# Kernel optimization log

Measured on AMD Instinct MI355X. Metric: run time of the kernel, lower is better.

## Reference

```python
import jax, jax.numpy as jnp
import numpy as np

# dims
BB, T, D_IN = 16, 2048, 64
D = 512          # hidden_dim (d_model)
DI = 2 * D       # d_inner (expand=2)
N = 16           # d_state
DC = 4           # d_conv
R = D // 16      # dt_rank = 32
L = 3            # n_layer
D_OUT = 128


def setup_inputs() -> dict:
    key = jax.random.key(0)
    ks = jax.random.split(key, 10)
    g = lambda k, shape, s: (jax.random.normal(k, shape, jnp.float32) * s)
    A_log = jnp.tile(jnp.log(jnp.arange(1, N + 1, dtype=jnp.float32))[None, None, :], (L, DI, 1))
    return {
        "x": g(ks[0], (BB, T, D_IN), 1.0),
        "Wi": g(ks[1], (D, D_IN), 0.05), "bi": jnp.zeros((D,), jnp.float32),
        "Win": g(ks[2], (L, 2 * DI, D), 0.02),
        "convw": g(ks[3], (L, DI, DC), 0.2), "convb": jnp.zeros((L, DI), jnp.float32),
        "Wx": g(ks[4], (L, R + 2 * N, DI), 0.02),
        "Wdt": g(ks[5], (L, DI, R), 0.05), "bdt": jnp.full((L, DI), -1.0, jnp.float32),
        "A_log": A_log, "Dp": jnp.ones((L, DI), jnp.float32),
        "Wout": g(ks[6], (L, D, DI), 0.02),
        "Wo": g(ks[7], (D_OUT, D), 0.05), "bo": jnp.zeros((D_OUT,), jnp.float32),
    }


def _selective_scan(u, delta, A, Bm, Cm, Dv):
    # u, delta: [B,T,DI]; A: [DI,N]; Bm, Cm: [B,T,N]; Dv: [DI]
    def step(h, inp):
        d_t, u_t, B_t, C_t = inp  # [B,DI],[B,DI],[B,N],[B,N]
        dA = jnp.exp(d_t[:, :, None] * A)                      # [B,DI,N]
        h = dA * h + (d_t * u_t)[:, :, None] * B_t[:, None, :]  # [B,DI,N]
        y = jnp.einsum('bdn,bn->bd', h, C_t)
        return h, y

    h0 = jnp.zeros((u.shape[0], u.shape[2], A.shape[1]), u.dtype)
    xs = (delta.transpose(1, 0, 2), u.transpose(1, 0, 2),
          Bm.transpose(1, 0, 2), Cm.transpose(1, 0, 2))
    _, ys = jax.lax.scan(step, h0, xs)
    return ys.transpose(1, 0, 2) + u * Dv


def _mamba_layer(x, Win, cw, cb, Wx, Wdt, bdt, A_log, Dv, Wout):
    xz = x @ Win.T                      # [B,T,2*DI]
    xin, z = jnp.split(xz, 2, axis=-1)
    # causal depthwise conv1d
    xc = jax.lax.conv_general_dilated(
        xin.transpose(0, 2, 1), cw[:, None, :], (1,), [(DC - 1, 0)],
        feature_group_count=DI, dimension_numbers=('NCH', 'OIH', 'NCH'))
    u = jax.nn.silu((xc + cb[None, :, None]).transpose(0, 2, 1))  # [B,T,DI]
    dbc = u @ Wx.T                      # [B,T,R+2N]
    dt, Bm, Cm = dbc[..., :R], dbc[..., R:R + N], dbc[..., R + N:]
    delta = jax.nn.softplus(dt @ Wdt.T + bdt)
    A = -jnp.exp(A_log)
    y = _selective_scan(u, delta, A, Bm, Cm, Dv)
    return (y * jax.nn.silu(z)) @ Wout.T


def reference(x, Wi, bi, Win, convw, convb, Wx, Wdt, bdt, A_log, Dp, Wout, Wo, bo):
    h = x @ Wi.T + bi
    for l in range(L):
        h = _mamba_layer(h, Win[l], convw[l], convb[l], Wx[l], Wdt[l], bdt[l],
                         A_log[l], Dp[l], Wout[l])
    return jnp.tanh(h @ Wo.T + bo)  # [B,T,output_dim]
```

## Files before the change

### kernel.cpp

```cpp
#include <hip/hip_runtime.h>
#include <hip/hip_bf16.h>

#define BB_ 16
#define T_ 2048
#define DIN_ 64
#define D_ 512
#define DI_ 1024
#define N_ 16
#define DC_ 4
#define R_ 32
#define L_ 3
#define DOUT_ 128
#define CL_ 64
#define NCH_ (T_ / CL_)

typedef __attribute__((ext_vector_type(8))) _Float16 f16x8;
typedef __attribute__((ext_vector_type(4))) float f32x4;

__device__ __forceinline__ float silu_f(float x) { return x / (1.f + __expf(-x)); }

__device__ __forceinline__ float softplus_f(float t) {
    return fmaxf(t, 0.f) + __logf(1.f + __expf(-fabsf(t)));
}

__device__ __forceinline__ unsigned short f2h(float f) {
    union { _Float16 h; unsigned short u; } c;
    c.h = (_Float16)f;
    return c.u;
}

__device__ __forceinline__ float h2f(unsigned short u) {
    union { unsigned short u; _Float16 h; } c;
    c.u = u;
    return (float)c.h;
}

__device__ __forceinline__ void gload_lds16(const unsigned short* g,
                                            unsigned short* l) {
    __builtin_amdgcn_global_load_lds(
        (const __attribute__((address_space(1))) void*)g,
        (__attribute__((address_space(3))) void*)l, 16, 0, 0);
}

__device__ __forceinline__ float decode_scale(unsigned int bits) {
    if (bits == 0u) return 1.f;
    const int E = (int)(bits >> 23) & 0xFF;
    return __uint_as_float((unsigned)(265 - E) << 23);
}

__device__ __forceinline__ uint4 pack8(float4 lo, float4 hi, float s) {
    union { uint4 u; unsigned short h[8]; } r;
    r.h[0] = f2h(lo.x * s); r.h[1] = f2h(lo.y * s);
    r.h[2] = f2h(lo.z * s); r.h[3] = f2h(lo.w * s);
    r.h[4] = f2h(hi.x * s); r.h[5] = f2h(hi.y * s);
    r.h[6] = f2h(hi.z * s); r.h[7] = f2h(hi.w * s);
    return r.u;
}

__device__ __forceinline__ const float* wregion(
    int r, const float* Win, const float* Wout, const float* Wx,
    const float* Wo, size_t* n4)
{
    if (r < 3)       { *n4 = 262144; return Win  + (size_t)r * 1048576; }
    else if (r < 6)  { *n4 = 131072; return Wout + (size_t)(r - 3) * 524288; }
    else if (r == 6) { *n4 = 16384;  return Wo; }
    else             { *n4 = 16384;  return Wx  + (size_t)(r - 7) * 65536; }
}

__global__ __launch_bounds__(256) void amax_all(
    const float* __restrict__ Win, const float* __restrict__ Wout,
    const float* __restrict__ Wx, const float* __restrict__ Wo,
    unsigned int* __restrict__ scales)
{
    size_t n4;
    const float* p = wregion(blockIdx.z, Win, Wout, Wx, Wo, &n4);
    float m = 0.f;
    for (size_t i = (size_t)blockIdx.x * 256 + threadIdx.x; i < n4;
         i += (size_t)gridDim.x * 256) {
        const float4 v = ((const float4*)p)[i];
        m = fmaxf(m, fmaxf(fmaxf(fabsf(v.x), fabsf(v.y)),
                           fmaxf(fabsf(v.z), fabsf(v.w))));
    }
#pragma unroll
    for (int off = 32; off; off >>= 1) m = fmaxf(m, __shfl_down(m, off));
    __shared__ float sm[4];
    if ((threadIdx.x & 63) == 0) sm[threadIdx.x >> 6] = m;
    __syncthreads();
    if (threadIdx.x == 0) {
        const float b = fmaxf(fmaxf(sm[0], sm[1]), fmaxf(sm[2], sm[3]));
        atomicMax(scales + blockIdx.z, __float_as_uint(b));
    }
}

__global__ __launch_bounds__(256) void cast_all(
    const float* __restrict__ Win, const float* __restrict__ Wout,
    const float* __restrict__ Wx, const float* __restrict__ Wo,
    unsigned short* __restrict__ WinH, unsigned short* __restrict__ WoutH,
    unsigned short* __restrict__ WxH, unsigned short* __restrict__ WoH,
    const unsigned int* __restrict__ scales)
{
    const int r = blockIdx.z;
    size_t n4;
    const float* p = wregion(r, Win, Wout, Wx, Wo, &n4);
    unsigned short* o;
    if (r < 3)       o = WinH  + (size_t)r * 1048576;
    else if (r < 6)  o = WoutH + (size_t)(r - 3) * 524288;
    else if (r == 6) o = WoH;
    else             o = WxH   + (size_t)(r - 7) * 65536;
    const float s = decode_scale(scales[r]);
    for (size_t i = (size_t)blockIdx.x * 256 + threadIdx.x; i < n4;
         i += (size_t)gridDim.x * 256) {
        const float4 v = ((const float4*)p)[i];
        ((ushort4*)o)[i] = make_ushort4(f2h(v.x * s), f2h(v.y * s),
                                        f2h(v.z * s), f2h(v.w * s));
    }
}

__global__ __launch_bounds__(256) void winrow_kernel(
    const float* __restrict__ Win, unsigned int* __restrict__ scales)
{
    const int l = blockIdx.z;
    const int row = blockIdx.x * 4 + (threadIdx.x >> 6);
    const int lane = threadIdx.x & 63;
    const float* W = Win + (size_t)l * 2 * DI_ * D_ + (size_t)row * D_ + lane * 8;
    float s = 0.f;
#pragma unroll
    for (int k = 0; k < 8; k += 4) {
        const float4 v = *(const float4*)(W + k);
        s += fabsf(v.x) + fabsf(v.y) + fabsf(v.z) + fabsf(v.w);
    }
#pragma unroll
    for (int off = 32; off; off >>= 1) s += __shfl_down(s, off);
    if (lane == 0) atomicMax(scales + 26 + l, __float_as_uint(s));
}

__global__ __launch_bounds__(256) void ubound_kernel(
    const float* __restrict__ cw, const float* __restrict__ cb,
    const unsigned int* __restrict__ hslot,
    const unsigned int* __restrict__ wbslot,
    unsigned int* __restrict__ uslot)
{
    const float amx = __uint_as_float(*hslot) * __uint_as_float(*wbslot);
    float m = 0.f;
    for (int c = threadIdx.x; c < DI_; c += 256) {
        const float4 w = *(const float4*)(cw + (size_t)c * 4);
        const float sw = fabsf(w.x) + fabsf(w.y) + fabsf(w.z) + fabsf(w.w);
        m = fmaxf(m, fabsf(cb[c]) + sw * amx);
    }
#pragma unroll
    for (int off = 32; off; off >>= 1) m = fmaxf(m, __shfl_down(m, off));
    __shared__ float sm[4];
    if ((threadIdx.x & 63) == 0) sm[threadIdx.x >> 6] = m;
    __syncthreads();
    if (threadIdx.x == 0) {
        const float b = fmaxf(fmaxf(sm[0], sm[1]), fmaxf(sm[2], sm[3]));
        atomicMax(uslot, __float_as_uint(b));
    }
}

template<int ACT>
__global__ __launch_bounds__(256) void gemm_f32a_t128(
    const float* __restrict__ A, int lda,
    const unsigned short* __restrict__ B, int ldb,
    const float* __restrict__ bias,
    float* __restrict__ C, int ldc, int K,
    const unsigned int* __restrict__ sa, const unsigned int* __restrict__ sb,
    unsigned int* __restrict__ oamax)
{
    __shared__ __align__(16) unsigned short As[128 * 32];
    __shared__ __align__(16) unsigned short Bs[2][128 * 32];
    const int tid  = threadIdx.x;
    const int lane = tid & 63;
    const int w    = tid >> 6;
    const int wr   = (w >> 1) << 6;
    const int wc   = (w & 1) << 6;
    const int l15  = lane & 15, l4 = lane >> 4;
    const int row0 = blockIdx.y << 7, col0 = blockIdx.x << 7;
    const int tq   = tid >> 2;
    const int tr   = (tid & 3) << 3;

    const float sA  = decode_scale(*sa);
    const float inv = (1.f / sA) * (1.f / decode_scale(*sb));

    const float* Ar0 = A + (size_t)(row0 + tq) * lda + tr;
    const float* Ar1 = A + (size_t)(row0 + 64 + tq) * lda + tr;
    const unsigned short* Br0 = B + (size_t)(col0 + tq) * ldb + tr;
    const unsigned short* Br1 = B + (size_t)(col0 + 64 + tq) * ldb + tr;

    f32x4 acc[4][4];
#pragma unroll
    for (int m = 0; m < 4; ++m)
#pragma unroll
        for (int n = 0; n < 4; ++n) acc[m][n] = (f32x4){0.f, 0.f, 0.f, 0.f};

    float4 a0lo = *(const float4*)(Ar0), a0hi = *(const float4*)(Ar0 + 4);
    float4 a1lo = *(const float4*)(Ar1), a1hi = *(const float4*)(Ar1 + 4);
    gload_lds16(Br0, &Bs[0][tq * 32 + tr]);
    gload_lds16(Br1, &Bs[0][(64 + tq) * 32 + tr]);

    int cur = 0;
    for (int k0 = 0; k0 < K; k0 += 32) {
        __syncthreads();
        *(uint4*)&As[tq * 32 + tr]        = pack8(a0lo, a0hi, sA);
        *(uint4*)&As[(64 + tq) * 32 + tr] = pack8(a1lo, a1hi, sA);
        __syncthreads();

        if (k0 + 32 < K) {
            gload_lds16(Br0 + k0 + 32, &Bs[cur ^ 1][tq * 32 + tr]);
            gload_lds16(Br1 + k0 + 32, &Bs[cur ^ 1][(64 + tq) * 32 + tr]);
            a0lo = *(const float4*)(Ar0 + k0 + 32);
            a0hi = *(const float4*)(Ar0 + k0 + 36);
            a1lo = *(const float4*)(Ar1 + k0 + 32);
            a1hi = *(const float4*)(Ar1 + k0 + 36);
        }

        f16x8 af[4], bfr[4];
#pragma unroll
        for (int m = 0; m < 4; ++m)
            af[m] = *(const f16x8*)&As[(wr + m * 16 + l15) * 32 + l4 * 8];
#pragma unroll
        for (int n = 0; n < 4; ++n)
            bfr[n] = *(const f16x8*)&Bs[cur][(wc + n * 16 + l15) * 32 + l4 * 8];
#pragma unroll
        for (int m = 0; m < 4; ++m)
#pragma unroll
            for (int n = 0; n < 4; ++n)
                acc[m][n] = __builtin_amdgcn_mfma_f32_16x16x32_f16(
                    af[m], bfr[n], acc[m][n], 0, 0, 0);
        cur ^= 1;
    }

    float am = 0.f;
#pragma unroll
    for (int n = 0; n < 4; ++n) {
        const int col = col0 + wc + n * 16 + l15;
        float bc = 0.f;
        if (ACT == 3) bc = bias[col];
#pragma unroll
        for (int m = 0; m < 4; ++m) {
            const int rowb = row0 + wr + m * 16 + (l4 << 2);
#pragma unroll
            for (int r = 0; r < 4; ++r) {
                float v = acc[m][n][r] * inv;
                if (ACT == 3) v = tanhf(v + bc);
                C[(size_t)(rowb + r) * ldc + col] = v;
                am = fmaxf(am, fabsf(v));
            }
        }
    }
    if (oamax) {
#pragma unroll
        for (int off = 32; off; off >>= 1) am = fmaxf(am, __shfl_down(am, off));
        if (lane == 0) atomicMax(oamax, __float_as_uint(am));
    }
}

__global__ __launch_bounds__(256) void gemm_f16_t64n(
    const unsigned short* __restrict__ A, int lda,
    const unsigned short* __restrict__ B, int ldb,
    float* __restrict__ C, int ldc, int K,
    const unsigned int* __restrict__ sa, const unsigned int* __restrict__ sb)
{
    __shared__ __align__(16) unsigned short As[128 * 32];
    __shared__ __align__(16) unsigned short Bs[64 * 32];
    const int tid  = threadIdx.x;
    const int lane = tid & 63;
    const int w    = tid >> 6;
    const int l15  = lane & 15, l4 = lane >> 4;
    const int row0 = blockIdx.y << 7;
    const int tq   = tid >> 2;
    const int tr   = (tid & 3) << 3;

    const float inv = (1.f / decode_scale(*sa)) * (1.f / decode_scale(*sb));

    const unsigned short* Ar0 = A + (size_t)(row0 + tq) * lda + tr;
    const unsigned short* Ar1 = A + (size_t)(row0 + 64 + tq) * lda + tr;
    const unsigned short* Br  = B + (size_t)tq * ldb + tr;

    f32x4 acc[2][4];
#pragma unroll
    for (int m = 0; m < 2; ++m)
#pragma unroll
        for (int n = 0; n < 4; ++n) acc[m][n] = (f32x4){0.f, 0.f, 0.f, 0.f};

    uint4 av0 = *(const uint4*)(Ar0);
    uint4 av1 = *(const uint4*)(Ar1);
    uint4 bv  = *(const uint4*)(Br);

    for (int k0 = 0; k0 < K; k0 += 32) {
        __syncthreads();
        *(uint4*)&As[tq * 32 + tr]        = av0;
        *(uint4*)&As[(64 + tq) * 32 + tr] = av1;
        *(uint4*)&Bs[tq * 32 + tr]        = bv;
        __syncthreads();

        if (k0 + 32 < K) {
            av0 = *(const uint4*)(Ar0 + k0 + 32);
            av1 = *(const uint4*)(Ar1 + k0 + 32);
            bv  = *(const uint4*)(Br  + k0 + 32);
        }

        f16x8 af[2], bfr[4];
#pragma unroll
        for (int m = 0; m < 2; ++m)
            af[m] = *(const f16x8*)&As[(w * 32 + m * 16 + l15) * 32 + l4 * 8];
#pragma unroll
        for (int n = 0; n < 4; ++n)
            bfr[n] = *(const f16x8*)&Bs[(n * 16 + l15) * 32 + l4 * 8];
#pragma unroll
        for (int m = 0; m < 2; ++m)
#pragma unroll
            for (int n = 0; n < 4; ++n)
                acc[m][n] = __builtin_amdgcn_mfma_f32_16x16x32_f16(
                    af[m], bfr[n], acc[m][n], 0, 0, 0);
    }

#pragma unroll
    for (int n = 0; n < 4; ++n) {
        const int col = n * 16 + l15;
#pragma unroll
        for (int m = 0; m < 2; ++m) {
            const int rowb = row0 + w * 32 + m * 16 + (l4 << 2);
#pragma unroll
            for (int r = 0; r < 4; ++r)
                C[(size_t)(rowb + r) * ldc + col] = acc[m][n][r] * inv;
        }
    }
}

__global__ __launch_bounds__(256) void gemm_in(
    const float* __restrict__ A, int lda,
    const float* __restrict__ B, int ldb,
    const float* __restrict__ bias,
    float* __restrict__ C, int ldc, int K,
    unsigned int* __restrict__ oamax)
{
    __shared__ __align__(16) float As[8][128];
    __shared__ __align__(16) float Bs[8][128];
    const int tid  = threadIdx.x;
    const int row0 = blockIdx.y << 7;
    const int col0 = blockIdx.x << 7;
    const int tx = tid & 15, ty = tid >> 4;

    float acc[8][8];
#pragma unroll
    for (int i = 0; i < 8; ++i)
#pragma unroll
        for (int j = 0; j < 8; ++j) acc[i][j] = 0.f;

    const int arow = tid >> 1;
    const int acol = (tid & 1) << 2;
    const float* Ap = A + (size_t)(row0 + arow) * lda + acol;
    const float* Bp = B + (size_t)(col0 + arow) * ldb + acol;

    for (int k0 = 0; k0 < K; k0 += 8) {
        const float4 av = *(const float4*)(Ap + k0);
        const float4 bv = *(const float4*)(Bp + k0);
        __syncthreads();
        As[acol + 0][arow] = av.x; As[acol + 1][arow] = av.y;
        As[acol + 2][arow] = av.z; As[acol + 3][arow] = av.w;
        Bs[acol + 0][arow] = bv.x; Bs[acol + 1][arow] = bv.y;
        Bs[acol + 2][arow] = bv.z; Bs[acol + 3][arow] = bv.w;
        __syncthreads();
#pragma unroll
        for (int k = 0; k < 8; ++k) {
            float a[8], b[8];
            *(float4*)&a[0] = *(const float4*)&As[k][ty << 3];
            *(float4*)&a[4] = *(const float4*)&As[k][(ty << 3) + 4];
            *(float4*)&b[0] = *(const float4*)&Bs[k][tx << 3];
            *(float4*)&b[4] = *(const float4*)&Bs[k][(tx << 3) + 4];
#pragma unroll
            for (int i = 0; i < 8; ++i)
#pragma unroll
                for (int j = 0; j < 8; ++j)
                    acc[i][j] = fmaf(a[i], b[j], acc[i][j]);
        }
    }

    float bv8[8];
#pragma unroll
    for (int j = 0; j < 8; ++j) bv8[j] = bias[col0 + (tx << 3) + j];

    float am = 0.f;
#pragma unroll
    for (int i = 0; i < 8; ++i) {
        float v[8];
#pragma unroll
        for (int j = 0; j < 8; ++j) {
            v[j] = acc[i][j] + bv8[j];
            am = fmaxf(am, fabsf(v[j]));
        }
        float* Cp = C + (size_t)(row0 + (ty << 3) + i) * ldc + col0 + (tx << 3);
        *(float4*)(Cp)     = make_float4(v[0], v[1], v[2], v[3]);
        *(float4*)(Cp + 4) = make_float4(v[4], v[5], v[6], v[7]);
    }
#pragma unroll
    for (int off = 32; off; off >>= 1) am = fmaxf(am, __shfl_down(am, off));
    if ((tid & 63) == 0) atomicMax(oamax, __float_as_uint(am));
}

__global__ __launch_bounds__(256) void conv_silu_kernel(
    const float* __restrict__ xz, const float* __restrict__ cw,
    const float* __restrict__ cb, unsigned short* __restrict__ u,
    size_t total4, const unsigned int* __restrict__ uslot)
{
    const float s = decode_scale(*uslot);
    for (size_t i = (size_t)blockIdx.x * 256 + threadIdx.x; i < total4;
         i += (size_t)gridDim.x * 256) {
        const size_t e = i * 4;
        const int c = (int)(e & (DI_ - 1));
        const size_t m = e >> 10;
        const int t = (int)(m & (T_ - 1));
        const float* xr = xz + m * 2048 + c;
        const float4 zero = make_float4(0.f, 0.f, 0.f, 0.f);
        const float4 x0 = (t >= 3) ? *(const float4*)(xr - 3 * 2048) : zero;
        const float4 x1 = (t >= 2) ? *(const float4*)(xr - 2 * 2048) : zero;
        const float4 x2 = (t >= 1) ? *(const float4*)(xr - 1 * 2048) : zero;
        const float4 x3 = *(const float4*)(xr);
        const float4 cbv = *(const float4*)(cb + c);
        const float4 w0 = *(const float4*)(cw + (size_t)c * 4);
        const float4 w1 = *(const float4*)(cw + (size_t)(c + 1) * 4);
        const float4 w2 = *(const float4*)(cw + (size_t)(c + 2) * 4);
        const float4 w3 = *(const float4*)(cw + (size_t)(c + 3) * 4);
        float4 r;
        r.x = silu_f(fmaf(x3.x, w0.w, fmaf(x2.x, w0.z, fmaf(x1.x, w0.y, fmaf(x0.x, w0.x, cbv.x)))));
        r.y = silu_f(fmaf(x3.y, w1.w, fmaf(x2.y, w1.z, fmaf(x1.y, w1.y, fmaf(x0.y, w1.x, cbv.y)))));
        r.z = silu_f(fmaf(x3.z, w2.w, fmaf(x2.z, w2.z, fmaf(x1.z, w2.y, fmaf(x0.z, w2.x, cbv.z)))));
        r.w = silu_f(fmaf(x3.w, w3.w, fmaf(x2.w, w3.z, fmaf(x1.w, w3.y, fmaf(x0.w, w3.x, cbv.w)))));
        *(ushort4*)(u + e) = make_ushort4(f2h(r.x * s), f2h(r.y * s),
                                          f2h(r.z * s), f2h(r.w * s));
    }
}


__device__ __forceinline__ bool geo_check(const float* a2) {
    bool ok = true;
#pragma unroll
    for (int n = 1; n < N_; ++n)
        ok = ok && (fabsf(a2[n] - a2[0] * (n + 1)) <=
                    1e-5f * fmaxf(1.f, fabsf(a2[n])));
    return ok;
}

__global__ __launch_bounds__(256) void scan_pass1(
    const unsigned short* __restrict__ u, const float* __restrict__ dbc,
    const float* __restrict__ A_log_l, const float* __restrict__ Wdt_l,
    const float* __restrict__ bdt_l, const unsigned int* __restrict__ uslot,
    float* __restrict__ SDL, float* __restrict__ S)
{
    __shared__ __align__(16) float sAll[CL_][64];
    const int tid = threadIdx.x;
    const int b = blockIdx.x, ch = blockIdx.z;
    const int d = (blockIdx.y << 8) + tid;

    float a2[N_], hs[N_];
#pragma unroll
    for (int n = 0; n < N_; ++n) {
        a2[n] = -__expf(A_log_l[d * N_ + n]) * 1.44269504f;
        hs[n] = 0.f;
    }
    const bool geo = geo_check(a2);
    const float invU = 1.f / decode_scale(*uslot);
    float wdt[32];
#pragma unroll
    for (int k = 0; k < 32; k += 4)
        *(float4*)&wdt[k] = *(const float4*)(Wdt_l + (size_t)d * 32 + k);
    const float bdt_d = bdt_l[d];

    const size_t base64 = ((size_t)b * T_ + (size_t)ch * CL_) * 64;
    float* sflat = &sAll[0][0];
    for (int i = tid; i < CL_ * 64; i += 256) sflat[i] = dbc[base64 + i];
    __syncthreads();

    float sdl = 0.f;
    if (geo) {
        for (int tt = 0; tt < CL_; ++tt) {
            float t = bdt_d;
#pragma unroll
            for (int k = 0; k < 32; k += 4) {
                const float4 dv = *(const float4*)&sAll[tt][k];
                t = fmaf(dv.x, wdt[k + 0], t);
                t = fmaf(dv.y, wdt[k + 1], t);
                t = fmaf(dv.z, wdt[k + 2], t);
                t = fmaf(dv.w, wdt[k + 3], t);
            }
            const float dl = softplus_f(t);
            sdl += dl;
            const size_t m = (size_t)b * T_ + ch * CL_ + tt;
            const float du = dl * (h2f(u[m * DI_ + d]) * invU);
            const float r = exp2f(dl * a2[0]);
            float dA = r;
#pragma unroll
            for (int n = 0; n < N_; ++n) {
                hs[n] = fmaf(dA, hs[n], du * sAll[tt][32 + n]);
                dA *= r;
            }
        }
    } else {
        for (int tt = 0; tt < CL_; ++tt) {
            float t = bdt_d;
#pragma unroll
            for (int k = 0; k < 32; k += 4) {
                const float4 dv = *(const float4*)&sAll[tt][k];
                t = fmaf(dv.x, wdt[k + 0], t);
                t = fmaf(dv.y, wdt[k + 1], t);
                t = fmaf(dv.z, wdt[k + 2], t);
                t = fmaf(dv.w, wdt[k + 3], t);
            }
            const float dl = softplus_f(t);
            sdl += dl;
            const size_t m = (size_t)b * T_ + ch * CL_ + tt;
            const float du = dl * (h2f(u[m * DI_ + d]) * invU);
#pragma unroll
            for (int n = 0; n < N_; ++n) {
                const float dA = exp2f(dl * a2[n]);
                hs[n] = fmaf(dA, hs[n], du * sAll[tt][32 + n]);
            }
        }
    }
    SDL[(size_t)((b * NCH_ + ch) << 10) + d] = sdl;
#pragma unroll
    for (int n = 0; n < N_; ++n) {
        const size_t idx = (size_t)(((b * NCH_ + ch) * N_ + n) << 10) + d;
        S[idx] = hs[n];
    }
}

__global__ __launch_bounds__(256) void scan_carry(
    const float* __restrict__ SDL, float* __restrict__ S,
    const float* __restrict__ A_log_l)
{
    const size_t gid = (size_t)blockIdx.x * 256 + threadIdx.x;
    const int d = (int)(gid & 1023);
    const int n = (int)((gid >> 10) & 15);
    const int b = (int)(gid >> 14);
    const float a2n = -__expf(A_log_l[d * N_ + n]) * 1.44269504f;
    float hc = 0.f;
    for (int ch = 0; ch < NCH_; ++ch) {
        const float sdl = SDL[(size_t)((b * NCH_ + ch) << 10) + d];
        const float p = exp2f(sdl * a2n);
        const size_t idx = (size_t)(((b * NCH_ + ch) * N_ + n) << 10) + d;
        const float s = S[idx];
        S[idx] = hc;
        hc = fmaf(p, hc, s);
    }
}

__global__ __launch_bounds__(256) void scan_pass3(
    float* __restrict__ xz, const unsigned short* __restrict__ u,
    const float* __restrict__ dbc, const float* __restrict__ A_log_l,
    const float* __restrict__ Wdt_l, const float* __restrict__ bdt_l,
    const float* __restrict__ Dp_l, const unsigned int* __restrict__ uslot,
    const float* __restrict__ S, unsigned int* __restrict__ gmax)
{
    __shared__ __align__(16) float sAll[CL_][64];
    const int tid = threadIdx.x;
    const int b = blockIdx.x, ch = blockIdx.z;
    const int d = (blockIdx.y << 8) + tid;

    float a2[N_], hs[N_];
#pragma unroll
    for (int n = 0; n < N_; ++n) {
        a2[n] = -__expf(A_log_l[d * N_ + n]) * 1.44269504f;
        hs[n] = S[(size_t)(((b * NCH_ + ch) * N_ + n) << 10) + d];
    }
    const bool geo = geo_check(a2);
    const float invU = 1.f / decode_scale(*uslot);
    float wdt[32];
#pragma unroll
    for (int k = 0; k < 32; k += 4)
        *(float4*)&wdt[k] = *(const float4*)(Wdt_l + (size_t)d * 32 + k);
    const float bdt_d = bdt_l[d];
    const float Dpd = Dp_l[d];

    const size_t base64 = ((size_t)b * T_ + (size_t)ch * CL_) * 64;
    float* sflat = &sAll[0][0];
    for (int i = tid; i < CL_ * 64; i += 256) sflat[i] = dbc[base64 + i];
    __syncthreads();

    float gm = 0.f;
    if (geo) {
        for (int tt = 0; tt < CL_; ++tt) {
            float t = bdt_d;
#pragma unroll
            for (int k = 0; k < 32; k += 4) {
                const float4 dv = *(const float4*)&sAll[tt][k];
                t = fmaf(dv.x, wdt[k + 0], t);
                t = fmaf(dv.y, wdt[k + 1], t);
                t = fmaf(dv.z, wdt[k + 2], t);
                t = fmaf(dv.w, wdt[k + 3], t);
            }
            const float dl = softplus_f(t);
            const size_t m = (size_t)b * T_ + ch * CL_ + tt;
            const float uv = h2f(u[m * DI_ + d]) * invU;
            const float du = dl * uv;
            const float r = exp2f(dl * a2[0]);
            float dA = r;
            float yv = 0.f;
#pragma unroll
            for (int n = 0; n < N_; ++n) {
                hs[n] = fmaf(dA, hs[n], du * sAll[tt][32 + n]);
                yv = fmaf(hs[n], sAll[tt][48 + n], yv);
                dA *= r;
            }
            yv = fmaf(uv, Dpd, yv);
            const float g = yv * silu_f(xz[m * 2048 + DI_ + d]);
            xz[m * 2048 + d] = g;
            gm = fmaxf(gm, fabsf(g));
        }
    } else {
        for (int tt = 0; tt < CL_; ++tt) {
            float t = bdt_d;
#pragma unroll
            for (int k = 0; k < 32; k += 4) {
                const float4 dv = *(const float4*)&sAll[tt][k];
                t = fmaf(dv.x, wdt[k + 0], t);
                t = fmaf(dv.y, wdt[k + 1], t);
                t = fmaf(dv.z, wdt[k + 2], t);
                t = fmaf(dv.w, wdt[k + 3], t);
            }
            const float dl = softplus_f(t);
            const size_t m = (size_t)b * T_ + ch * CL_ + tt;
            const float uv = h2f(u[m * DI_ + d]) * invU;
            const float du = dl * uv;
            float yv = 0.f;
#pragma unroll
            for (int n = 0; n < N_; ++n) {
                const float dA = exp2f(dl * a2[n]);
                hs[n] = fmaf(dA, hs[n], du * sAll[tt][32 + n]);
                yv = fmaf(hs[n], sAll[tt][48 + n], yv);
            }
            yv = fmaf(uv, Dpd, yv);
            const float g = yv * silu_f(xz[m * 2048 + DI_ + d]);
            xz[m * 2048 + d] = g;
            gm = fmaxf(gm, fabsf(g));
        }
    }
#pragma unroll
    for (int off = 32; off; off >>= 1) gm = fmaxf(gm, __shfl_down(gm, off));
    if ((tid & 63) == 0) atomicMax(gmax, __float_as_uint(gm));
}

extern "C" void kernel_launch(void* const* d_in, const int* in_sizes, int n_in,
                              void* d_out, int out_size, void* d_ws, size_t ws_size,
                              hipStream_t stream) {
    const float* x     = (const float*)d_in[0];
    const float* Wi    = (const float*)d_in[1];
    const float* bi    = (const float*)d_in[2];
    const float* Win   = (const float*)d_in[3];
    const float* convw = (const float*)d_in[4];
    const float* convb = (const float*)d_in[5];
    const float* Wx    = (const float*)d_in[6];
    const float* Wdt   = (const float*)d_in[7];
    const float* bdt   = (const float*)d_in[8];
    const float* A_log = (const float*)d_in[9];
    const float* Dp    = (const float*)d_in[10];
    const float* Wout  = (const float*)d_in[11];
    const float* Wo    = (const float*)d_in[12];
    const float* bo    = (const float*)d_in[13];
    float* out = (float*)d_out;

    const size_t rowf = 3648;
    const size_t wextra =
        (3 * 1048576 + 3 * 524288 + 65536 + 3 * 65536) / 2 + 32;
    int CB = BB_;
    while (CB > 1 && ((size_t)CB * T_ * rowf + wextra) * sizeof(float) > ws_size) CB >>= 1;
    const size_t Mc = (size_t)CB * T_;

    const dim3 blk(256);
    const int rowTiles = (int)(Mc / 128);

    float* ws   = (float*)d_ws;
    float* xz   = ws;
    float* uf   = xz + Mc * 2048;
    unsigned short* ub = (unsigned short*)uf;
    float* dbc  = uf + Mc * 512;
    float* hPS  = dbc + Mc * 64;
    float* hb   = hPS;
    float* Sdl  = hPS;
    float* Sbuf = hPS + Mc * 16;
    unsigned short* WinH  = (unsigned short*)(hPS + Mc * 512);
    unsigned short* WoutH = WinH + 3 * 1048576;
    unsigned short* WoH   = WoutH + 3 * 524288;
    unsigned short* WxH   = WoH + 65536;
    unsigned int* scales  = (unsigned int*)(WxH + 3 * 65536);

    hipMemsetAsync(scales, 0, 32 * sizeof(unsigned int), stream);

    amax_all<<<dim3(128, 1, 10), blk, 0, stream>>>(Win, Wout, Wx, Wo, scales);
    winrow_kernel<<<dim3(512, 1, 3), blk, 0, stream>>>(Win, scales);
    cast_all<<<dim3(64, 1, 10), blk, 0, stream>>>(
        Win, Wout, Wx, Wo, WinH, WoutH, WxH, WoH, scales);

    for (int c = 0; c < BB_ / CB; ++c) {
        const float* x_c = x + (size_t)c * Mc * DIN_;
        float* out_c     = out + (size_t)c * Mc * DOUT_;

        hipMemsetAsync(scales + 10, 0, 16 * sizeof(unsigned int), stream);

        gemm_in<<<dim3(D_ / 128, rowTiles), blk, 0, stream>>>(
            x_c, DIN_, Wi, DIN_, bi, hb, D_, DIN_, scales + 10);

        for (int l = 0; l < L_; ++l) {
            const float* cw_l   = convw + (size_t)l * DI_ * DC_;
            const float* cb_l   = convb + (size_t)l * DI_;
            const float* Wdt_l  = Wdt  + (size_t)l * DI_ * R_;
            const float* bdt_l  = bdt  + (size_t)l * DI_;
            const float* Alog_l = A_log + (size_t)l * DI_ * N_;
            const float* Dp_l   = Dp   + (size_t)l * DI_;

            ubound_kernel<<<dim3(1), blk, 0, stream>>>(
                cw_l, cb_l, scales + 10 + l, scales + 26 + l, scales + 20 + l);

            gemm_f32a_t128<0><<<dim3(2048 / 128, rowTiles), blk, 0, stream>>>(
                hb, D_, WinH + (size_t)l * 1048576, D_, nullptr,
                xz, 2048, D_, scales + 10 + l, scales + l, nullptr);

            conv_silu_kernel<<<dim3(2048), blk, 0, stream>>>(
                xz, cw_l, cb_l, ub, Mc * DI_ / 4, scales + 20 + l);

            gemm_f16_t64n<<<dim3(1, rowTiles), blk, 0, stream>>>(
                ub, DI_, WxH + (size_t)l * 65536, DI_, dbc, 64, DI_,
                scales + 20 + l, scales + 7 + l);

            scan_pass1<<<dim3(CB, DI_ / 256, NCH_), blk, 0, stream>>>(
                ub, dbc, Alog_l, Wdt_l, bdt_l, scales + 20 + l, Sdl, Sbuf);
            scan_carry<<<dim3(CB * 64), blk, 0, stream>>>(Sdl, Sbuf, Alog_l);
            scan_pass3<<<dim3(CB, DI_ / 256, NCH_), blk, 0, stream>>>(
                xz, ub, dbc, Alog_l, Wdt_l, bdt_l, Dp_l, scales + 20 + l,
                Sbuf, scales + 14 + l);

            gemm_f32a_t128<0><<<dim3(D_ / 128, rowTiles), blk, 0, stream>>>(
                xz, 2048, WoutH + (size_t)l * 524288, DI_, nullptr,
                hb, D_, DI_, scales + 14 + l, scales + 3 + l, scales + 11 + l);
        }

        gemm_f32a_t128<3><<<dim3(DOUT_ / 128, rowTiles), blk, 0, stream>>>(
            hb, D_, WoH, D_, bo, out_c, DOUT_, D_,
            scales + 13, scales + 6, nullptr);
    }
}
```

Before: 2.582 ms.

## Store in-projection output xz as scaled fp16 with separate gate buffer

The in-projection GEMM now writes xz as scaled fp16 instead of fp32, using a bound derived from the input and weight maxima. The conv/silu and scan pass-3 kernels read and dequantize it. Pass 3 now writes the gated output to a separate fp32 buffer instead of overwriting xz in place. This halves the xz store and load traffic, which is the largest intermediate, at the cost of fp16 rounding on the activations and the z gate.

```diff
diff --git a/kernel.cpp b/kernel.cpp
--- a/kernel.cpp
+++ b/kernel.cpp
@@ -138,14 +138,15 @@
     const float* __restrict__ cw, const float* __restrict__ cb,
     const unsigned int* __restrict__ hslot,
     const unsigned int* __restrict__ wbslot,
-    unsigned int* __restrict__ uslot)
-{
-    const float amx = __uint_as_float(*hslot) * __uint_as_float(*wbslot);
+    unsigned int* __restrict__ xzbslot, unsigned int* __restrict__ uslot)
+{
+    const float xzb = __uint_as_float(*hslot) * __uint_as_float(*wbslot);
+    if (threadIdx.x == 0) atomicMax(xzbslot, __float_as_uint(xzb));
     float m = 0.f;
     for (int c = threadIdx.x; c < DI_; c += 256) {
         const float4 w = *(const float4*)(cw + (size_t)c * 4);
         const float sw = fabsf(w.x) + fabsf(w.y) + fabsf(w.z) + fabsf(w.w);
-        m = fmaxf(m, fabsf(cb[c]) + sw * amx);
+        m = fmaxf(m, fabsf(cb[c]) + sw * xzb);
     }
 #pragma unroll
     for (int off = 32; off; off >>= 1) m = fmaxf(m, __shfl_down(m, off));
@@ -158,14 +159,14 @@
     }
 }
 
-template<int ACT>
+template<int ACT, int OUTH>
 __global__ __launch_bounds__(256) void gemm_f32a_t128(
     const float* __restrict__ A, int lda,
     const unsigned short* __restrict__ B, int ldb,
     const float* __restrict__ bias,
-    float* __restrict__ C, int ldc, int K,
+    void* __restrict__ Cv, int ldc, int K,
     const unsigned int* __restrict__ sa, const unsigned int* __restrict__ sb,
-    unsigned int* __restrict__ oamax)
+    const unsigned int* __restrict__ so, unsigned int* __restrict__ oamax)
 {
     __shared__ __align__(16) unsigned short As[128 * 32];
     __shared__ __align__(16) unsigned short Bs[2][128 * 32];
@@ -181,6 +182,7 @@
 
     const float sA  = decode_scale(*sa);
     const float inv = (1.f / sA) * (1.f / decode_scale(*sb));
+    const float sOut = OUTH ? decode_scale(*so) : 1.f;
 
     const float* Ar0 = A + (size_t)(row0 + tq) * lda + tr;
     const float* Ar1 = A + (size_t)(row0 + 64 + tq) * lda + tr;
@@ -243,12 +245,17 @@
             for (int r = 0; r < 4; ++r) {
                 float v = acc[m][n][r] * inv;
                 if (ACT == 3) v = tanhf(v + bc);
-                C[(size_t)(rowb + r) * ldc + col] = v;
-                am = fmaxf(am, fabsf(v));
-            }
-        }
-    }
-    if (oamax) {
+                if (OUTH) {
+                    ((unsigned short*)Cv)[(size_t)(rowb + r) * ldc + col] =
+                        f2h(v * sOut);
+                } else {
+                    ((float*)Cv)[(size_t)(rowb + r) * ldc + col] = v;
+                    am = fmaxf(am, fabsf(v));
+                }
+            }
+        }
+    }
+    if (!OUTH && oamax) {
 #pragma unroll
         for (int off = 32; off; off >>= 1) am = fmaxf(am, __shfl_down(am, off));
         if (lane == 0) atomicMax(oamax, __float_as_uint(am));
@@ -400,10 +407,12 @@
 }
 
 __global__ __launch_bounds__(256) void conv_silu_kernel(
-    const float* __restrict__ xz, const float* __restrict__ cw,
+    const unsigned short* __restrict__ xzh, const float* __restrict__ cw,
     const float* __restrict__ cb, unsigned short* __restrict__ u,
-    size_t total4, const unsigned int* __restrict__ uslot)
-{
+    size_t total4, const unsigned int* __restrict__ xzbslot,
+    const unsigned int* __restrict__ uslot)
+{
+    const float invX = 1.f / decode_scale(*xzbslot);
     const float s = decode_scale(*uslot);
     for (size_t i = (size_t)blockIdx.x * 256 + threadIdx.x; i < total4;
          i += (size_t)gridDim.x * 256) {
@@ -411,24 +420,42 @@
         const int c = (int)(e & (DI_ - 1));
         const size_t m = e >> 10;
         const int t = (int)(m & (T_ - 1));
-        const float* xr = xz + m * 2048 + c;
-        const float4 zero = make_float4(0.f, 0.f, 0.f, 0.f);
-        const float4 x0 = (t >= 3) ? *(const float4*)(xr - 3 * 2048) : zero;
-        const float4 x1 = (t >= 2) ? *(const float4*)(xr - 2 * 2048) : zero;
-        const float4 x2 = (t >= 1) ? *(const float4*)(xr - 1 * 2048) : zero;
-        const float4 x3 = *(const float4*)(xr);
+        const unsigned short* xr = xzh + m * 2048 + c;
+        float x[4][4];
+#pragma unroll
+        for (int k = 0; k < 4; ++k) {
+            const int dt = 3 - k;
+            if (t >= dt) {
+                const ushort4 xv = *(const ushort4*)(xr - (size_t)dt * 2048);
+                x[k][0] = h2f(xv.x) * invX; x[k][1] = h2f(xv.y) * invX;
+                x[k][2] = h2f(xv.z) * invX; x[k][3] = h2f(xv.w) * invX;
+            } else {
+                x[k][0] = x[k][1] = x[k][2] = x[k][3] = 0.f;
+            }
+        }
         const float4 cbv = *(const float4*)(cb + c);
-        const float4 w0 = *(const float4*)(cw + (size_t)c * 4);
-        const float4 w1 = *(const float4*)(cw + (size_t)(c + 1) * 4);
-        const float4 w2 = *(const float4*)(cw + (size_t)(c + 2) * 4);
-        const float4 w3 = *(const float4*)(cw + (size_t)(c + 3) * 4);
-        float4 r;
-        r.x = silu_f(fmaf(x3.x, w0.w, fmaf(x2.x, w0.z, fmaf(x1.x, w0.y, fmaf(x0.x, w0.x, cbv.x)))));
-        r.y = silu_f(fmaf(x3.y, w1.w, fmaf(x2.y, w1.z, fmaf(x1.y, w1.y, fmaf(x0.y, w1.x, cbv.y)))));
-        r.z = silu_f(fmaf(x3.z, w2.w, fmaf(x2.z, w2.z, fmaf(x1.z, w2.y, fmaf(x0.z, w2.x, cbv.z)))));
-        r.w = silu_f(fmaf(x3.w, w3.w, fmaf(x2.w, w3.z, fmaf(x1.w, w3.y, fmaf(x0.w, w3.x, cbv.w)))));
-        *(ushort4*)(u + e) = make_ushort4(f2h(r.x * s), f2h(r.y * s),
-                                          f2h(r.z * s), f2h(r.w * s));
+        ushort4 o;
+        {
+            const float4 w = *(const float4*)(cw + (size_t)c * 4);
+            o.x = f2h(silu_f(fmaf(x[3][0], w.w, fmaf(x[2][0], w.z,
+                     fmaf(x[1][0], w.y, fmaf(x[0][0], w.x, cbv.x))))) * s);
+        }
+        {
+            const float4 w = *(const float4*)(cw + (size_t)(c + 1) * 4);
+            o.y = f2h(silu_f(fmaf(x[3][1], w.w, fmaf(x[2][1], w.z,
+                     fmaf(x[1][1], w.y, fmaf(x[0][1], w.x, cbv.y))))) * s);
+        }
+        {
+            const float4 w = *(const float4*)(cw + (size_t)(c + 2) * 4);
+            o.z = f2h(silu_f(fmaf(x[3][2], w.w, fmaf(x[2][2], w.z,
+                     fmaf(x[1][2], w.y, fmaf(x[0][2], w.x, cbv.z))))) * s);
+        }
+        {
+            const float4 w = *(const float4*)(cw + (size_t)(c + 3) * 4);
+            o.w = f2h(silu_f(fmaf(x[3][3], w.w, fmaf(x[2][3], w.z,
+                     fmaf(x[1][3], w.y, fmaf(x[0][3], w.x, cbv.w))))) * s);
+        }
+        *(ushort4*)(u + e) = o;
     }
 }
 
@@ -547,10 +574,12 @@
 }
 
 __global__ __launch_bounds__(256) void scan_pass3(
-    float* __restrict__ xz, const unsigned short* __restrict__ u,
-    const float* __restrict__ dbc, const float* __restrict__ A_log_l,
-    const float* __restrict__ Wdt_l, const float* __restrict__ bdt_l,
-    const float* __restrict__ Dp_l, const unsigned int* __restrict__ uslot,
+    const unsigned short* __restrict__ xzh, float* __restrict__ g,
+    const unsigned short* __restrict__ u, const float* __restrict__ dbc,
+    const float* __restrict__ A_log_l, const float* __restrict__ Wdt_l,
+    const float* __restrict__ bdt_l, const float* __restrict__ Dp_l,
+    const unsigned int* __restrict__ xzbslot,
+    const unsigned int* __restrict__ uslot,
     const float* __restrict__ S, unsigned int* __restrict__ gmax)
 {
     __shared__ __align__(16) float sAll[CL_][64];
@@ -565,6 +594,7 @@
         hs[n] = S[(size_t)(((b * NCH_ + ch) * N_ + n) << 10) + d];
     }
     const bool geo = geo_check(a2);
+    const float invX = 1.f / decode_scale(*xzbslot);
     const float invU = 1.f / decode_scale(*uslot);
     float wdt[32];
 #pragma unroll
@@ -604,9 +634,10 @@
                 dA *= r;
             }
             yv = fmaf(uv, Dpd, yv);
-            const float g = yv * silu_f(xz[m * 2048 + DI_ + d]);
-            xz[m * 2048 + d] = g;
-            gm = fmaxf(gm, fabsf(g));
+            const float zv = h2f(xzh[m * 2048 + DI_ + d]) * invX;
+            const float gv = yv * silu_f(zv);
+            g[m * DI_ + d] = gv;
+            gm = fmaxf(gm, fabsf(gv));
         }
     } else {
         for (int tt = 0; tt < CL_; ++tt) {
@@ -631,9 +662,10 @@
                 yv = fmaf(hs[n], sAll[tt][48 + n], yv);
             }
             yv = fmaf(uv, Dpd, yv);
-            const float g = yv * silu_f(xz[m * 2048 + DI_ + d]);
-            xz[m * 2048 + d] = g;
-            gm = fmaxf(gm, fabsf(g));
+            const float zv = h2f(xzh[m * 2048 + DI_ + d]) * invX;
+            const float gv = yv * silu_f(zv);
+            g[m * DI_ + d] = gv;
+            gm = fmaxf(gm, fabsf(gv));
         }
     }
 #pragma unroll
@@ -671,10 +703,10 @@
     const int rowTiles = (int)(Mc / 128);
 
     float* ws   = (float*)d_ws;
-    float* xz   = ws;
-    float* uf   = xz + Mc * 2048;
-    unsigned short* ub = (unsigned short*)uf;
-    float* dbc  = uf + Mc * 512;
+    unsigned short* xzh = (unsigned short*)ws;
+    float* gbuf = ws + Mc * 1024;
+    unsigned short* ub = (unsigned short*)(gbuf + Mc * 1024);
+    float* dbc  = gbuf + Mc * 1024 + Mc * 512;
     float* hPS  = dbc + Mc * 64;
     float* hb   = hPS;
     float* Sdl  = hPS;
@@ -710,14 +742,17 @@
             const float* Dp_l   = Dp   + (size_t)l * DI_;
 
             ubound_kernel<<<dim3(1), blk, 0, stream>>>(
-                cw_l, cb_l, scales + 10 + l, scales + 26 + l, scales + 20 + l);
-
-            gemm_f32a_t128<0><<<dim3(2048 / 128, rowTiles), blk, 0, stream>>>(
+                cw_l, cb_l, scales + 10 + l, scales + 26 + l,
+                scales + 17 + l, scales + 20 + l);
+
+            gemm_f32a_t128<0, 1><<<dim3(2048 / 128, rowTiles), blk, 0, stream>>>(
                 hb, D_, WinH + (size_t)l * 1048576, D_, nullptr,
-                xz, 2048, D_, scales + 10 + l, scales + l, nullptr);
+                xzh, 2048, D_, scales + 10 + l, scales + l,
+                scales + 17 + l, nullptr);
 
             conv_silu_kernel<<<dim3(2048), blk, 0, stream>>>(
-                xz, cw_l, cb_l, ub, Mc * DI_ / 4, scales + 20 + l);
+                xzh, cw_l, cb_l, ub, Mc * DI_ / 4,
+                scales + 17 + l, scales + 20 + l);
 
             gemm_f16_t64n<<<dim3(1, rowTiles), blk, 0, stream>>>(
                 ub, DI_, WxH + (size_t)l * 65536, DI_, dbc, 64, DI_,
@@ -727,16 +762,17 @@
                 ub, dbc, Alog_l, Wdt_l, bdt_l, scales + 20 + l, Sdl, Sbuf);
             scan_carry<<<dim3(CB * 64), blk, 0, stream>>>(Sdl, Sbuf, Alog_l);
             scan_pass3<<<dim3(CB, DI_ / 256, NCH_), blk, 0, stream>>>(
-                xz, ub, dbc, Alog_l, Wdt_l, bdt_l, Dp_l, scales + 20 + l,
-                Sbuf, scales + 14 + l);
-
-            gemm_f32a_t128<0><<<dim3(D_ / 128, rowTiles), blk, 0, stream>>>(
-                xz, 2048, WoutH + (size_t)l * 524288, DI_, nullptr,
-                hb, D_, DI_, scales + 14 + l, scales + 3 + l, scales + 11 + l);
-        }
-
-        gemm_f32a_t128<3><<<dim3(DOUT_ / 128, rowTiles), blk, 0, stream>>>(
+                xzh, gbuf, ub, dbc, Alog_l, Wdt_l, bdt_l, Dp_l,
+                scales + 17 + l, scales + 20 + l, Sbuf, scales + 14 + l);
+
+            gemm_f32a_t128<0, 0><<<dim3(D_ / 128, rowTiles), blk, 0, stream>>>(
+                gbuf, DI_, WoutH + (size_t)l * 524288, DI_, nullptr,
+                hb, D_, DI_, scales + 14 + l, scales + 3 + l,
+                nullptr, scales + 11 + l);
+        }
+
+        gemm_f32a_t128<3, 0><<<dim3(DOUT_ / 128, rowTiles), blk, 0, stream>>>(
             hb, D_, WoH, D_, bo, out_c, DOUT_, D_,
-            scales + 13, scales + 6, nullptr);
-    }
-}
+            scales + 13, scales + 6, nullptr, nullptr);
+    }
+}
```

After: 2.182 ms (median of 2 runs). 1.18x faster.
